# Performance work log

Hardware: AMD Instinct MI355X
Metric: run time of the kernel (lower is better)

The kernel has to match this reference:

```python
import jax, jax.numpy as jnp
import numpy as np
from jax import lax

N_G, E_G, E_LG = 100000, 400000, 1200000
N_T, E_T, E_LGT = 50000, 100000, 300000
D_F, D_MSG_G = 64, 128
VOCAB, D_EMB, D_MSG_T = 780, 128, 128
N_ITERS_G, N_ITERS_T = 4, 4
SCALE = 0.05  # keep relu/sum chains numerically tame over iterations


def setup_inputs() -> dict:
    key = jax.random.key(0)
    ks = jax.random.split(key, 32)
    f32 = jnp.float32
    w = lambda k, sh: jax.random.normal(k, sh, f32) * SCALE
    return {
        "G_f": jax.random.normal(ks[0], (N_G, D_F), f32),
        "G_ef": jax.random.normal(ks[1], (E_G, D_F), f32),
        "G_src": jax.random.randint(ks[2], (E_G,), 0, N_G, jnp.int32),
        "G_dst": jax.random.randint(ks[3], (E_G,), 0, N_G, jnp.int32),
        "G_lg_src": jax.random.randint(ks[4], (E_LG,), 0, E_G, jnp.int32),
        "G_lg_dst": jax.random.randint(ks[5], (E_LG,), 0, E_G, jnp.int32),
        "T_id": jax.random.randint(ks[6], (N_T,), 0, VOCAB, jnp.int32),
        "T_src": jax.random.randint(ks[7], (E_T,), 0, N_T, jnp.int32),
        "T_dst": jax.random.randint(ks[8], (E_T,), 0, N_T, jnp.int32),
        "T_lg_src": jax.random.randint(ks[9], (E_LGT,), 0, E_T, jnp.int32),
        "T_lg_dst": jax.random.randint(ks[10], (E_LGT,), 0, E_T, jnp.int32),
        "embeddings": jax.random.normal(ks[11], (VOCAB, D_EMB), f32),
        "W1": w(ks[12], (D_F, D_MSG_G)),
        "W2": w(ks[13], (D_F, D_MSG_G)),
        "W3": w(ks[14], (D_MSG_G, D_MSG_G)),
        "U1_G": w(ks[15], (D_F, D_MSG_G)),
        "U2_G": w(ks[16], (D_MSG_G, D_MSG_G)),
        "Wz": w(ks[17], (D_EMB, D_MSG_T)),
        "Uz": w(ks[18], (D_MSG_T, D_MSG_T)),
        "Wr": w(ks[19], (D_EMB, D_MSG_T)),
        "Ur": w(ks[20], (D_MSG_T, D_MSG_T)),
        "Wh": w(ks[21], (D_EMB, D_MSG_T)),
        "Uh": w(ks[22], (D_MSG_T, D_MSG_T)),
        "U1_T": w(ks[23], (D_EMB, D_MSG_T)),
        "U2_T": w(ks[24], (D_MSG_T, D_MSG_T)),
    }


def reference(G_f, G_ef, G_src, G_dst, G_lg_src, G_lg_dst,
              T_id, T_src, T_dst, T_lg_src, T_lg_dst,
              embeddings, W1, W2, W3, U1_G, U2_G,
              Wz, Uz, Wr, Ur, Wh, Uh, U1_T, U2_T):
    seg = jax.ops.segment_sum

    # ---- molecule graph G: loopy-BP MLP messages on the line graph ----
    f_src_G = G_f[G_src]                               # [E_G, D_F] copy_src
    base_G = f_src_G @ W1 + G_ef @ W2                  # loop-invariant part of g1_G

    def stepG(msg, _):
        sum_msg = seg(msg[G_lg_src], G_lg_dst, num_segments=E_G)
        return jax.nn.relu(base_G + sum_msg @ W3), None

    msgG0 = jnp.zeros((E_G, D_MSG_G), G_f.dtype)
    msgG, _ = lax.scan(stepG, msgG0, None, length=N_ITERS_G)

    # readout g2_G: sum edge msgs into dst nodes
    sG = seg(msgG, G_dst, num_segments=N_G)
    x_G = jax.nn.relu(G_f @ U1_G + sG @ U2_G)          # [N_G, D_MSG_G]

    # ---- junction tree T: GRU messages on the tree line graph ----
    f_T = embeddings[T_id]                             # one-hot id @ embeddings
    f_src_T = f_T[T_src]                               # [E_T, D_EMB]
    xz, xr, xh = f_src_T @ Wz, f_src_T @ Wr, f_src_T @ Wh

    def stepT(msg, _):
        s = seg(msg[T_lg_src], T_lg_dst, num_segments=E_T)
        z = jax.nn.sigmoid(xz + s @ Uz)
        r = jax.nn.sigmoid(xr + s @ Ur)
        h = jnp.tanh(xh + (r * s) @ Uh)
        return (1.0 - z) * s + z * h, None

    msgT0 = jnp.zeros((E_T, D_MSG_T), f_T.dtype)
    msgT, _ = lax.scan(stepT, msgT0, None, length=N_ITERS_T)

    sT = seg(msgT, T_dst, num_segments=N_T)
    x_T = jax.nn.relu(f_T @ U1_T + sT @ U2_T)          # [N_T, D_MSG_T]

    # concat node readouts (same width) so output is a single array
    return jnp.concatenate([x_G, x_T], axis=0)         # [N_G+N_T, 128]
```

## Files before the change

kernel.cpp:

```cpp
#include <hip/hip_runtime.h>

#define NG 100000
#define EG 400000
#define ELG 1200000
#define NT 50000
#define ET 100000
#define ELGT 300000

#define GEG ((EG + 63) / 64)
#define GET ((ET + 63) / 64)
#define GNG ((NG + 63) / 64)
#define GNT ((NT + 63) / 64)

#define SEG1 EG
#define SEG2 (EG + NG)
#define SEG3 (EG + NG + ET)
#define NSEG_ALL (EG + NG + ET + NT)
#define NE_ALL (ELG + EG + ELGT + ET)
#define NE_PAD (NE_ALL + 3 * NSEG_ALL + 64)

typedef unsigned short u16;
typedef unsigned int u32;
typedef __attribute__((ext_vector_type(8))) short bf16x8;
typedef __attribute__((ext_vector_type(4))) float f32x4;

#define TILE_B 16384

__device__ __forceinline__ float bflo(u32 p){ return __uint_as_float(p << 16); }
__device__ __forceinline__ float bfhi(u32 p){ return __uint_as_float(p & 0xffff0000u); }
__device__ __forceinline__ float bf2f(u16 h){ return __uint_as_float(((u32)h) << 16); }
__device__ __forceinline__ u16 f2bf(float f){
  u32 u = __float_as_uint(f);
  u32 r = u + 0x7fffu + ((u >> 16) & 1u);
  return (u16)(r >> 16);
}
__device__ __forceinline__ float sigm(float x){ return 1.0f / (1.0f + __expf(-x)); }
__device__ __forceinline__ float tanh_(float x){ return 2.0f / (1.0f + __expf(-2.0f * x)) - 1.0f; }
__device__ __forceinline__ float relu_(float x){ return x > 0.0f ? x : 0.0f; }
__device__ __forceinline__ void wfence(){ __builtin_amdgcn_wave_barrier(); }

__device__ __forceinline__ int swz(int r, int c){ return r * 256 + (c ^ ((r & 7) << 4)); }

__device__ __forceinline__ void zero8(float v[8]){
  #pragma unroll
  for (int j = 0; j < 8; j++) v[j] = 0.f;
}
__device__ __forceinline__ uint4 pack8(const float v[8]){
  uint4 o;
  o.x = f2bf(v[0]) | ((u32)f2bf(v[1]) << 16);
  o.y = f2bf(v[2]) | ((u32)f2bf(v[3]) << 16);
  o.z = f2bf(v[4]) | ((u32)f2bf(v[5]) << 16);
  o.w = f2bf(v[6]) | ((u32)f2bf(v[7]) << 16);
  return o;
}
__device__ __forceinline__ uint2 pack4(const f32x4& a){
  uint2 o;
  o.x = (u32)f2bf(a[0]) | ((u32)f2bf(a[1]) << 16);
  o.y = (u32)f2bf(a[2]) | ((u32)f2bf(a[3]) << 16);
  return o;
}
__device__ __forceinline__ void unp4(uint2 u, float v[4]){
  v[0] = bflo(u.x); v[1] = bfhi(u.x); v[2] = bflo(u.y); v[3] = bfhi(u.y);
}
__device__ __forceinline__ bf16x8 packfrag(const float v[8]){
  union { uint4 u; bf16x8 b; } c; c.u = pack8(v); return c.b;
}
__device__ __forceinline__ bf16x8 zfrag(){
  union { uint4 u; bf16x8 b; } c; c.u = make_uint4(0, 0, 0, 0); return c.b;
}
__device__ __forceinline__ bf16x8 as_frag(uint4 u){
  union { uint4 u; bf16x8 b; } c; c.u = u; return c.b;
}

__global__ void k_sniff(const u32* __restrict__ g, int* __restrict__ flag){
  __shared__ int sh[2];
  if (threadIdx.x < 2) sh[threadIdx.x] = 0;
  __syncthreads();
  int c0 = 0, c1 = 0;
  for (int i = 0; i < 16; i++){
    u32 w = g[threadIdx.x * 16 + i];
    u32 lo = w & 0xFFFFu;
    if (lo == 0u) c0++;
    else { u32 e = (lo >> 7) & 0xFFu; if (e >= 96u && e <= 144u) c1++; }
  }
  atomicAdd(&sh[0], c0); atomicAdd(&sh[1], c1);
  __syncthreads();
  if (threadIdx.x == 0) *flag = (sh[0] < 512 && sh[1] > 2048) ? 1 : 0;
}

__global__ void k_cvt_all(const void* p0, const void* p1, const void* p2, const void* p3,
                          const void* p4, const void* p5, const void* p6, const void* p7,
                          const void* p8, const void* p9, const void* p10, const void* p11,
                          const void* p12, float* __restrict__ wm, const int* __restrict__ flagp){
  int i = blockIdx.x * 256 + threadIdx.x;
  if (i >= 188416) return;
  const int offs[14] = {0,8192,16384,32768,40960,57344,73728,90112,106496,122880,139264,155648,172032,188416};
  const void* ps[13] = {p0,p1,p2,p3,p4,p5,p6,p7,p8,p9,p10,p11,p12};
  int w = 0;
  while (i >= offs[w + 1]) w++;
  int li = i - offs[w];
  wm[i] = (*flagp) ? bf2f(((const u16*)ps[w])[li]) : ((const float*)ps[w])[li];
}

__global__ void k_mkfrag_all(const float* __restrict__ wm, u16* __restrict__ frag){
  const int wmo[13] = {0,8192,16384,32768,40960,57344,73728,90112,106496,122880,139264,155648,172032};
  const int nks[13] = {2,2,4,2,4,4,4,4,4,4,4,4,4};
  int b = blockIdx.x;
  int wi = 0, ks = b;
  while (ks >= nks[wi]){ ks -= nks[wi]; wi++; }
  const float* W = wm + wmo[wi];
  int nt = threadIdx.x >> 6, lane = threadIdx.x & 63;
  int kr = ks * 32 + ((lane >> 4) << 3);
  int col = nt * 16 + (lane & 15);
  u16* o = frag + (size_t)b * 4096 + nt * 512 + lane * 8;
  #pragma unroll
  for (int j = 0; j < 8; j++) o[j] = f2bf(W[(size_t)(kr + j) * 128 + col]);
}

__device__ __forceinline__ const void* rowdt(const void* mat, size_t row, int W, int bf){
  return bf ? (const void*)((const u16*)mat + row * (size_t)W)
            : (const void*)((const float*)mat + row * (size_t)W);
}
__device__ __forceinline__ void load8(const void* rowbase, int c8, int bf, float v[8]){
  if (bf){
    uint4 d = ((const uint4*)rowbase)[c8];
    v[0]=bflo(d.x); v[1]=bfhi(d.x); v[2]=bflo(d.y); v[3]=bfhi(d.y);
    v[4]=bflo(d.z); v[5]=bfhi(d.z); v[6]=bflo(d.w); v[7]=bfhi(d.w);
  } else {
    const float4* p = (const float4*)rowbase + (c8 << 1);
    float4 a = p[0], b = p[1];
    v[0]=a.x; v[1]=a.y; v[2]=a.z; v[3]=a.w; v[4]=b.x; v[5]=b.y; v[6]=b.z; v[7]=b.w;
  }
}

__global__ void k_hist_all(const int* __restrict__ Glgd, const int* __restrict__ Gd,
                           const int* __restrict__ Tlgd, const int* __restrict__ Td,
                           int* __restrict__ cnt){
  int e = blockIdx.x * 256 + threadIdx.x;
  if (e >= NE_ALL) return;
  int seg;
  if (e < ELG)                       seg = Glgd[e];
  else if (e < ELG + EG)             seg = SEG1 + Gd[e - ELG];
  else if (e < ELG + EG + ELGT)      seg = SEG2 + Tlgd[e - ELG - EG];
  else                               seg = SEG3 + Td[e - ELG - EG - ELGT];
  atomicAdd(&cnt[seg], 1);
}

__global__ void k_scan1(const int* __restrict__ cnt, int n, int* __restrict__ csum){
  int base = blockIdx.x * 4096, tid = threadIdx.x;
  int s = 0;
  for (int i = 0; i < 16; i++){
    int idx = base + i * 256 + tid;
    if (idx < n) s += (cnt[idx] + 3) & ~3;
  }
  __shared__ int red[4];
  for (int off = 32; off; off >>= 1) s += __shfl_down(s, off, 64);
  if ((tid & 63) == 0) red[tid >> 6] = s;
  __syncthreads();
  if (tid == 0) csum[blockIdx.x] = red[0] + red[1] + red[2] + red[3];
}

__global__ void k_scan2(int* csum, int nch, int* rowptr, int n){
  if (threadIdx.x == 0){
    int run = 0;
    for (int c = 0; c < nch; c++){ int t = csum[c]; csum[c] = run; run += t; }
    rowptr[n] = run;
  }
}

__global__ void k_scan3(const int* __restrict__ cnt, int n, const int* __restrict__ csum,
                        int* __restrict__ rowptr){
  __shared__ int buf[4096];
  __shared__ int tsum[256];
  int base = blockIdx.x * 4096, tid = threadIdx.x;
  for (int i = 0; i < 16; i++){
    int idx = base + i * 256 + tid;
    buf[i * 256 + tid] = (idx < n) ? ((cnt[idx] + 3) & ~3) : 0;
  }
  __syncthreads();
  int run = 0;
  for (int i = 0; i < 16; i++){ int v = buf[tid * 16 + i]; buf[tid * 16 + i] = run; run += v; }
  tsum[tid] = run;
  __syncthreads();
  for (int off = 1; off < 256; off <<= 1){
    int v = (tid >= off) ? tsum[tid - off] : 0;
    __syncthreads();
    tsum[tid] += v;
    __syncthreads();
  }
  int texcl = tsum[tid] - run;
  int cbase = csum[blockIdx.x];
  for (int i = 0; i < 16; i++){
    int idx = base + tid * 16 + i;
    if (idx < n) rowptr[idx] = cbase + texcl + buf[tid * 16 + i];
  }
}

__global__ void k_fill_all(const int* __restrict__ Glgd, const int* __restrict__ Glgs,
                           const int* __restrict__ Gd,
                           const int* __restrict__ Tlgd, const int* __restrict__ Tlgs,
                           const int* __restrict__ Td,
                           const int* __restrict__ rowptr, int* __restrict__ fill,
                           int* __restrict__ col){
  int e = blockIdx.x * 256 + threadIdx.x;
  if (e >= NE_ALL) return;
  int seg, srcv;
  if (e < ELG){                      seg = Glgd[e];                           srcv = Glgs[e]; }
  else if (e < ELG + EG){            int l = e - ELG;                         seg = SEG1 + Gd[l];   srcv = l; }
  else if (e < ELG + EG + ELGT){     int l = e - ELG - EG;                    seg = SEG2 + Tlgd[l]; srcv = Tlgs[l]; }
  else {                             int l = e - ELG - EG - ELGT;             seg = SEG3 + Td[l];   srcv = l; }
  int pos = atomicAdd(&fill[seg], 1);
  col[rowptr[seg] + pos] = srcv;
}

__global__ void k_fill_pad(const int* __restrict__ cnt, const int* __restrict__ rowptr,
                           int* __restrict__ col){
  int seg = blockIdx.x * 256 + threadIdx.x;
  if (seg >= NSEG_ALL) return;
  int dummy = (seg < SEG2) ? EG : ET;
  int start = rowptr[seg] + cnt[seg];
  int end = rowptr[seg + 1];
  for (int q = start; q < end; q++) col[q] = dummy;
}

__global__ void k_zero_dummy(u16* a, u16* b, u16* c, u16* d){
  int i = threadIdx.x;
  if (i < 128){
    a[(size_t)EG * 128 + i] = 0; b[(size_t)EG * 128 + i] = 0;
    c[(size_t)ET * 128 + i] = 0; d[(size_t)ET * 128 + i] = 0;
  }
}


__device__ __forceinline__ void acc8_add(float (&a)[8], uint4 d){
  a[0] += bflo(d.x); a[1] += bfhi(d.x);
  a[2] += bflo(d.y); a[3] += bfhi(d.y);
  a[4] += bflo(d.z); a[5] += bfhi(d.z);
  a[6] += bflo(d.w); a[7] += bfhi(d.w);
}

__device__ __forceinline__ void gather_accum(const int* __restrict__ rowptr,
    const int* __restrict__ colidx, const u16* __restrict__ msg,
    int row, int M, int kg, float (&acc)[4][8])
{
  #pragma unroll
  for (int ks = 0; ks < 4; ks++) zero8(acc[ks]);
  if (row >= M) return;
  int p = rowptr[row], pe = rowptr[row + 1];
  for (; p < pe; p += 4){
    int i0 = colidx[p], i1 = colidx[p + 1], i2 = colidx[p + 2], i3 = colidx[p + 3];
    const uint4* b0 = (const uint4*)(msg + (size_t)i0 * 128);
    const uint4* b1 = (const uint4*)(msg + (size_t)i1 * 128);
    const uint4* b2 = (const uint4*)(msg + (size_t)i2 * 128);
    const uint4* b3 = (const uint4*)(msg + (size_t)i3 * 128);
    uint4 v0[4], v1[4], v2[4], v3[4];
    #pragma unroll
    for (int ks = 0; ks < 4; ks++){
      v0[ks] = b0[ks * 4 + kg]; v1[ks] = b1[ks * 4 + kg];
      v2[ks] = b2[ks * 4 + kg]; v3[ks] = b3[ks * 4 + kg];
    }
    #pragma unroll
    for (int ks = 0; ks < 4; ks++){
      acc8_add(acc[ks], v0[ks]); acc8_add(acc[ks], v1[ks]);
      acc8_add(acc[ks], v2[ks]); acc8_add(acc[ks], v3[ks]);
    }
  }
}

template<int KS>
__device__ __forceinline__ void mma_f(const bf16x8* a, const u16* __restrict__ frag,
                                      f32x4 (&acc)[8])
{
  int lane = threadIdx.x & 63;
  #pragma unroll
  for (int ks = 0; ks < KS; ks++){
    const u16* fb = frag + (size_t)ks * 4096 + lane * 8;
    #pragma unroll
    for (int nt = 0; nt < 8; nt++){
      bf16x8 b = *(const bf16x8*)(fb + (size_t)nt * 512);
      acc[nt] = __builtin_amdgcn_mfma_f32_16x16x32_bf16(a[ks], b, acc[nt], 0, 0, 0);
    }
  }
}

#define INIT_ACC(A) { _Pragma("unroll") for (int n_=0;n_<8;n_++){ A[n_][0]=0.f; A[n_][1]=0.f; A[n_][2]=0.f; A[n_][3]=0.f; } }

__device__ __forceinline__ void repack_store(const char* __restrict__ tile,
    u16* __restrict__ dst, int row0, int M)
{
  int rl = threadIdx.x >> 2, q = threadIdx.x & 3;
  int grow = row0 + rl;
  if (grow < M){
    #pragma unroll
    for (int v = 0; v < 4; v++){
      uint4 d = *(const uint4*)(tile + swz(rl, (v * 4 + q) * 16));
      *(uint4*)(dst + (size_t)grow * 128 + (size_t)(v * 4 + q) * 8) = d;
    }
  }
}

__device__ __forceinline__ size_t fslot(int blk, int w, int nt){
  return ((((size_t)blk * 4 + w) * 8 + nt) * 64 + (threadIdx.x & 63)) * 4;
}

__device__ __forceinline__ void load_catfrag(const void* __restrict__ Gf,
    const void* __restrict__ Gef, const int* __restrict__ Gsrc,
    int arow, int kg, int bf, bf16x8 (&fC)[4])
{
  if (arow < EG){
    int sr = Gsrc[arow];
    const void* ra = rowdt(Gf, (size_t)sr, 64, bf);
    const void* rb = rowdt(Gef, (size_t)arow, 64, bf);
    float t[8];
    load8(ra, kg, bf, t);     fC[0] = packfrag(t);
    load8(ra, 4 + kg, bf, t); fC[1] = packfrag(t);
    load8(rb, kg, bf, t);     fC[2] = packfrag(t);
    load8(rb, 4 + kg, bf, t); fC[3] = packfrag(t);
  } else {
    #pragma unroll
    for (int ks = 0; ks < 4; ks++) fC[ks] = zfrag();
  }
}


__global__ __launch_bounds__(256, 4) void k_init(
    const void* __restrict__ Gf, const void* __restrict__ Gef, const int* __restrict__ Gsrc,
    const u16* __restrict__ fWcat, const int* __restrict__ flagp, u16* __restrict__ msgG,
    const void* __restrict__ emb, const int* __restrict__ Tid, const int* __restrict__ Tsrc,
    const u16* __restrict__ fWz, const u16* __restrict__ fWr, const u16* __restrict__ fWh,
    u16* __restrict__ xzf, u16* __restrict__ xrf, u16* __restrict__ xhf, u16* __restrict__ msgT)
{
  __shared__ char t0[TILE_B];
  int bf = *flagp;
  int lane = threadIdx.x & 63, w = threadIdx.x >> 6;
  int stripe = w * 16, kg = lane >> 4, m16 = lane & 15;
  if (blockIdx.x < GET){
    int blk = blockIdx.x, row0 = blk * 64, arow = row0 + stripe + m16;
    bf16x8 fE[4];
    if (arow < ET){
      int id = Tid[Tsrc[arow]];
      const void* rb = rowdt(emb, (size_t)id, 128, bf);
      #pragma unroll
      for (int ks = 0; ks < 4; ks++){
        float t[8]; load8(rb, ks * 4 + kg, bf, t); fE[ks] = packfrag(t);
      }
    } else {
      #pragma unroll
      for (int ks = 0; ks < 4; ks++) fE[ks] = zfrag();
    }
    f32x4 acc[8];
    uint2 zpk[8];
    INIT_ACC(acc);
    mma_f<4>(fE, fWz, acc);
    #pragma unroll
    for (int nt = 0; nt < 8; nt++){
      zpk[nt] = pack4(acc[nt]);
      *(uint2*)(xzf + fslot(blk, w, nt)) = zpk[nt];
    }
    INIT_ACC(acc);
    mma_f<4>(fE, fWr, acc);
    #pragma unroll
    for (int nt = 0; nt < 8; nt++)
      *(uint2*)(xrf + fslot(blk, w, nt)) = pack4(acc[nt]);
    INIT_ACC(acc);
    mma_f<4>(fE, fWh, acc);
    #pragma unroll
    for (int nt = 0; nt < 8; nt++){
      *(uint2*)(xhf + fslot(blk, w, nt)) = pack4(acc[nt]);
      float xzv[4]; unp4(zpk[nt], xzv);
      #pragma unroll
      for (int r = 0; r < 4; r++){
        int rt = stripe + (kg << 2) + r;
        int cb = nt * 32 + m16 * 2;
        *(u16*)(t0 + swz(rt, cb)) = f2bf(sigm(xzv[r]) * tanh_(acc[nt][r]));
      }
    }
    wfence();
    repack_store(t0, msgT, row0, ET);
  } else {
    int blk = blockIdx.x - GET, row0 = blk * 64, arow = row0 + stripe + m16;
    bf16x8 fC[4];
    load_catfrag(Gf, Gef, Gsrc, arow, kg, bf, fC);
    f32x4 acc[8]; INIT_ACC(acc);
    mma_f<4>(fC, fWcat, acc);
    #pragma unroll
    for (int nt = 0; nt < 8; nt++)
      #pragma unroll
      for (int r = 0; r < 4; r++){
        int rt = stripe + (kg << 2) + r;
        int cb = nt * 32 + m16 * 2;
        *(u16*)(t0 + swz(rt, cb)) = f2bf(relu_(acc[nt][r]));
      }
    wfence();
    repack_store(t0, msgG, row0, EG);
  }
}

__global__ __launch_bounds__(256, 4) void k_iter(
    const u16* __restrict__ msgInG, u16* __restrict__ msgOutG,
    const void* __restrict__ Gf, const void* __restrict__ Gef, const int* __restrict__ Gsrc,
    const int* __restrict__ rp, const int* __restrict__ col,
    const u16* __restrict__ fWcat, const u16* __restrict__ fW3, const int* __restrict__ flagp,
    const u16* __restrict__ msgInT, u16* __restrict__ msgOutT,
    const u16* __restrict__ fUz, const u16* __restrict__ fUr, const u16* __restrict__ fUh,
    const u16* __restrict__ xzf, const u16* __restrict__ xrf, const u16* __restrict__ xhf)
{
  __shared__ char t0[TILE_B];
  __shared__ char t1[TILE_B];
  int lane = threadIdx.x & 63, w = threadIdx.x >> 6;
  int stripe = w * 16, kg = lane >> 4, m16 = lane & 15;
  if (blockIdx.x < GET){
    int blk = blockIdx.x, row0 = blk * 64, arow = row0 + stripe + m16;
    float ga[4][8];
    gather_accum(rp + SEG2, col, msgInT, arow, ET, kg, ga);
    bf16x8 fS[4];
    #pragma unroll
    for (int ks = 0; ks < 4; ks++){
      uint4 pk = pack8(ga[ks]);
      *(uint4*)(t0 + swz(stripe + m16, ks * 64 + kg * 16)) = pk;
      fS[ks] = as_frag(pk);
    }
    f32x4 acc[8];
    INIT_ACC(acc);
    mma_f<4>(fS, fUr, acc);
    wfence();
    #pragma unroll
    for (int nt = 0; nt < 8; nt++){
      uint2 r4 = *(const uint2*)(xrf + fslot(blk, w, nt));
      float xrv[4]; unp4(r4, xrv);
      #pragma unroll
      for (int r = 0; r < 4; r++){
        int rt = stripe + (kg << 2) + r;
        int cb = nt * 32 + m16 * 2;
        float s = bf2f(*(const u16*)(t0 + swz(rt, cb)));
        float rr = sigm(xrv[r] + acc[nt][r]);
        *(u16*)(t1 + swz(rt, cb)) = f2bf(rr * s);
      }
    }
    wfence();
    bf16x8 fRS[4];
    #pragma unroll
    for (int ks = 0; ks < 4; ks++)
      fRS[ks] = *(const bf16x8*)(t1 + swz(stripe + m16, ks * 64 + kg * 16));
    INIT_ACC(acc);
    mma_f<4>(fRS, fUh, acc);
    wfence();
    #pragma unroll
    for (int nt = 0; nt < 8; nt++){
      uint2 h4 = *(const uint2*)(xhf + fslot(blk, w, nt));
      float xhv[4]; unp4(h4, xhv);
      #pragma unroll
      for (int r = 0; r < 4; r++){
        int rt = stripe + (kg << 2) + r;
        int cb = nt * 32 + m16 * 2;
        *(u16*)(t1 + swz(rt, cb)) = f2bf(tanh_(xhv[r] + acc[nt][r]));
      }
    }
    wfence();
    bf16x8 fS2[4];
    #pragma unroll
    for (int ks = 0; ks < 4; ks++)
      fS2[ks] = *(const bf16x8*)(t0 + swz(stripe + m16, ks * 64 + kg * 16));
    INIT_ACC(acc);
    mma_f<4>(fS2, fUz, acc);
    wfence();
    #pragma unroll
    for (int nt = 0; nt < 8; nt++){
      uint2 z4 = *(const uint2*)(xzf + fslot(blk, w, nt));
      float xzv[4]; unp4(z4, xzv);
      #pragma unroll
      for (int r = 0; r < 4; r++){
        int rt = stripe + (kg << 2) + r;
        int cb = nt * 32 + m16 * 2;
        float z = sigm(xzv[r] + acc[nt][r]);
        float s = bf2f(*(const u16*)(t0 + swz(rt, cb)));
        float h = bf2f(*(const u16*)(t1 + swz(rt, cb)));
        *(u16*)(t0 + swz(rt, cb)) = f2bf((1.f - z) * s + z * h);
      }
    }
    wfence();
    repack_store(t0, msgOutT, row0, ET);
  } else {
    int bf = *flagp;
    int blk = blockIdx.x - GET, row0 = blk * 64, arow = row0 + stripe + m16;
    float ga[4][8];
    gather_accum(rp, col, msgInG, arow, EG, kg, ga);
    bf16x8 fS[4];
    #pragma unroll
    for (int ks = 0; ks < 4; ks++) fS[ks] = packfrag(ga[ks]);
    bf16x8 fC[4];
    load_catfrag(Gf, Gef, Gsrc, arow, kg, bf, fC);
    f32x4 acc[8]; INIT_ACC(acc);
    mma_f<4>(fS, fW3, acc);
    mma_f<4>(fC, fWcat, acc);
    #pragma unroll
    for (int nt = 0; nt < 8; nt++)
      #pragma unroll
      for (int r = 0; r < 4; r++){
        int rt = stripe + (kg << 2) + r;
        int cb = nt * 32 + m16 * 2;
        *(u16*)(t0 + swz(rt, cb)) = f2bf(relu_(acc[nt][r]));
      }
    wfence();
    repack_store(t0, msgOutG, row0, EG);
  }
}

__global__ __launch_bounds__(256, 4) void k_readout(
    const void* __restrict__ Gf, const u16* __restrict__ msgG,
    const int* __restrict__ rp, const int* __restrict__ col,
    const u16* __restrict__ fU1G, const u16* __restrict__ fU2G,
    const void* __restrict__ emb, const int* __restrict__ Tid, const u16* __restrict__ msgT,
    const u16* __restrict__ fU1T, const u16* __restrict__ fU2T,
    const int* __restrict__ flagp, float* __restrict__ out)
{
  int bf = *flagp;
  int lane = threadIdx.x & 63, w = threadIdx.x >> 6;
  int stripe = w * 16, kg = lane >> 4, m16 = lane & 15;
  if (blockIdx.x < GNT){
    int row0 = blockIdx.x * 64, arow = row0 + stripe + m16;
    float ga[4][8];
    gather_accum(rp + SEG3, col, msgT, arow, NT, kg, ga);
    bf16x8 fS[4];
    #pragma unroll
    for (int ks = 0; ks < 4; ks++) fS[ks] = packfrag(ga[ks]);
    bf16x8 fE[4];
    if (arow < NT){
      int id = Tid[arow];
      const void* rb = rowdt(emb, (size_t)id, 128, bf);
      #pragma unroll
      for (int ks = 0; ks < 4; ks++){
        float t[8]; load8(rb, ks * 4 + kg, bf, t); fE[ks] = packfrag(t);
      }
    } else {
      #pragma unroll
      for (int ks = 0; ks < 4; ks++) fE[ks] = zfrag();
    }
    f32x4 acc[8]; INIT_ACC(acc);
    mma_f<4>(fS, fU2T, acc);
    mma_f<4>(fE, fU1T, acc);
    #pragma unroll
    for (int nt = 0; nt < 8; nt++)
      #pragma unroll
      for (int r = 0; r < 4; r++){
        int R = row0 + stripe + (kg << 2) + r;
        if (R < NT) out[(size_t)(NG + R) * 128 + nt * 16 + m16] = relu_(acc[nt][r]);
      }
  } else {
    int row0 = (blockIdx.x - GNT) * 64, arow = row0 + stripe + m16;
    float ga[4][8];
    gather_accum(rp + SEG1, col, msgG, arow, NG, kg, ga);
    bf16x8 fS[4];
    #pragma unroll
    for (int ks = 0; ks < 4; ks++) fS[ks] = packfrag(ga[ks]);
    bf16x8 fG[2];
    if (arow < NG){
      const void* ra = rowdt(Gf, (size_t)arow, 64, bf);
      float t[8];
      load8(ra, kg, bf, t);     fG[0] = packfrag(t);
      load8(ra, 4 + kg, bf, t); fG[1] = packfrag(t);
    } else { fG[0] = zfrag(); fG[1] = zfrag(); }
    f32x4 acc[8]; INIT_ACC(acc);
    mma_f<4>(fS, fU2G, acc);
    mma_f<2>(fG, fU1G, acc);
    #pragma unroll
    for (int nt = 0; nt < 8; nt++)
      #pragma unroll
      for (int r = 0; r < 4; r++){
        int R = row0 + stripe + (kg << 2) + r;
        if (R < NG) out[(size_t)R * 128 + nt * 16 + m16] = relu_(acc[nt][r]);
      }
  }
}

extern "C" void kernel_launch(void* const* d_in, const int* in_sizes, int n_in,
                              void* d_out, int out_size, void* d_ws, size_t ws_size,
                              hipStream_t stream)
{
  const void* G_f      = d_in[0];
  const void* G_ef     = d_in[1];
  const int*  G_src    = (const int*)d_in[2];
  const int*  G_dst    = (const int*)d_in[3];
  const int*  G_lg_src = (const int*)d_in[4];
  const int*  G_lg_dst = (const int*)d_in[5];
  const int*  T_id     = (const int*)d_in[6];
  const int*  T_src    = (const int*)d_in[7];
  const int*  T_dst    = (const int*)d_in[8];
  const int*  T_lg_src = (const int*)d_in[9];
  const int*  T_lg_dst = (const int*)d_in[10];
  const void* emb      = d_in[11];
  float* out = (float*)d_out;
  (void)in_sizes; (void)n_in; (void)out_size; (void)ws_size;

  size_t off = 0;
  auto alloc = [&](size_t bytes) -> char* {
    char* p = (char*)d_ws + off;
    off += (bytes + 255) & ~(size_t)255;
    return p;
  };

  int*   flag = (int*)alloc(256);
  float* wm   = (float*)alloc(sizeof(float) * 188416);
  u16*   frag = (u16*)alloc(2 * 46 * 4096);
  const u16* fWcat = frag;
  const u16* fW3   = frag + (size_t)4  * 4096;
  const u16* fU1G  = frag + (size_t)8  * 4096;
  const u16* fU2G  = frag + (size_t)10 * 4096;
  const u16* fWz   = frag + (size_t)14 * 4096;
  const u16* fUz   = frag + (size_t)18 * 4096;
  const u16* fWr   = frag + (size_t)22 * 4096;
  const u16* fUr   = frag + (size_t)26 * 4096;
  const u16* fWh   = frag + (size_t)30 * 4096;
  const u16* fUh   = frag + (size_t)34 * 4096;
  const u16* fU1T  = frag + (size_t)38 * 4096;
  const u16* fU2T  = frag + (size_t)42 * 4096;

  int* rp   = (int*)alloc(sizeof(int) * (NSEG_ALL + 1));
  int* col  = (int*)alloc(sizeof(int) * NE_PAD);
  int* cnt  = (int*)alloc(sizeof(int) * 2 * NSEG_ALL);
  int* csum = (int*)alloc(sizeof(int) * 256);
  u16* msgGA = (u16*)alloc((size_t)(EG + 1) * 128 * 2);
  u16* msgGB = (u16*)alloc((size_t)(EG + 1) * 128 * 2);
  u16* xzf   = (u16*)alloc((size_t)GET * 8192 * 2);
  u16* xrf   = (u16*)alloc((size_t)GET * 8192 * 2);
  u16* xhf   = (u16*)alloc((size_t)GET * 8192 * 2);
  u16* msgTA = (u16*)alloc((size_t)(ET + 1) * 128 * 2);
  u16* msgTB = (u16*)alloc((size_t)(ET + 1) * 128 * 2);

  k_sniff<<<1, 256, 0, stream>>>((const u32*)G_ef, flag);
  k_cvt_all<<<(188416 + 255) / 256, 256, 0, stream>>>(
      d_in[12], d_in[13], d_in[14], d_in[15], d_in[16], d_in[17], d_in[18],
      d_in[19], d_in[20], d_in[21], d_in[22], d_in[23], d_in[24], wm, flag);
  k_mkfrag_all<<<46, 512, 0, stream>>>(wm, frag);
  k_zero_dummy<<<1, 128, 0, stream>>>(msgGA, msgGB, msgTA, msgTB);

  hipMemsetAsync(cnt, 0, sizeof(int) * 2 * NSEG_ALL, stream);
  k_hist_all<<<(NE_ALL + 255) / 256, 256, 0, stream>>>(G_lg_dst, G_dst, T_lg_dst, T_dst, cnt);
  int nch = (NSEG_ALL + 4095) / 4096;
  k_scan1<<<nch, 256, 0, stream>>>(cnt, NSEG_ALL, csum);
  k_scan2<<<1, 64, 0, stream>>>(csum, nch, rp, NSEG_ALL);
  k_scan3<<<nch, 256, 0, stream>>>(cnt, NSEG_ALL, csum, rp);
  k_fill_all<<<(NE_ALL + 255) / 256, 256, 0, stream>>>(
      G_lg_dst, G_lg_src, G_dst, T_lg_dst, T_lg_src, T_dst, rp, cnt + NSEG_ALL, col);
  k_fill_pad<<<(NSEG_ALL + 255) / 256, 256, 0, stream>>>(cnt, rp, col);

  k_init<<<GET + GEG, 256, 0, stream>>>(G_f, G_ef, G_src, fWcat, flag, msgGA,
                                        emb, T_id, T_src, fWz, fWr, fWh, xzf, xrf, xhf, msgTA);
  k_iter<<<GET + GEG, 256, 0, stream>>>(msgGA, msgGB, G_f, G_ef, G_src, rp, col, fWcat, fW3, flag,
                                        msgTA, msgTB, fUz, fUr, fUh, xzf, xrf, xhf);
  k_iter<<<GET + GEG, 256, 0, stream>>>(msgGB, msgGA, G_f, G_ef, G_src, rp, col, fWcat, fW3, flag,
                                        msgTB, msgTA, fUz, fUr, fUh, xzf, xrf, xhf);
  k_iter<<<GET + GEG, 256, 0, stream>>>(msgGA, msgGB, G_f, G_ef, G_src, rp, col, fWcat, fW3, flag,
                                        msgTA, msgTB, fUz, fUr, fUh, xzf, xrf, xhf);
  k_readout<<<GNT + GNG, 256, 0, stream>>>(G_f, msgGB, rp, col, fU1G, fU2G,
                                           emb, T_id, msgTB, fU1T, fU2T, flag, out);
}
```

Before: 1.098 ms.

## Fold neighbor-sum gather into MFMA via distributivity; cut shared tile and use nontemporal stores

```diff
diff --git a/kernel.cpp b/kernel.cpp
--- a/kernel.cpp
+++ b/kernel.cpp
@@ -23,6 +23,7 @@
 typedef unsigned int u32;
 typedef __attribute__((ext_vector_type(8))) short bf16x8;
 typedef __attribute__((ext_vector_type(4))) float f32x4;
+typedef __attribute__((ext_vector_type(4))) u32 u32x4;
 
 #define TILE_B 16384
 
@@ -39,20 +40,13 @@
 __device__ __forceinline__ float relu_(float x){ return x > 0.0f ? x : 0.0f; }
 __device__ __forceinline__ void wfence(){ __builtin_amdgcn_wave_barrier(); }
 
+__device__ __forceinline__ void stnt4(void* p, uint4 d){
+  u32x4 v = {d.x, d.y, d.z, d.w};
+  __builtin_nontemporal_store(v, (u32x4*)p);
+}
+
 __device__ __forceinline__ int swz(int r, int c){ return r * 256 + (c ^ ((r & 7) << 4)); }
 
-__device__ __forceinline__ void zero8(float v[8]){
-  #pragma unroll
-  for (int j = 0; j < 8; j++) v[j] = 0.f;
-}
-__device__ __forceinline__ uint4 pack8(const float v[8]){
-  uint4 o;
-  o.x = f2bf(v[0]) | ((u32)f2bf(v[1]) << 16);
-  o.y = f2bf(v[2]) | ((u32)f2bf(v[3]) << 16);
-  o.z = f2bf(v[4]) | ((u32)f2bf(v[5]) << 16);
-  o.w = f2bf(v[6]) | ((u32)f2bf(v[7]) << 16);
-  return o;
-}
 __device__ __forceinline__ uint2 pack4(const f32x4& a){
   uint2 o;
   o.x = (u32)f2bf(a[0]) | ((u32)f2bf(a[1]) << 16);
@@ -62,14 +56,25 @@
 __device__ __forceinline__ void unp4(uint2 u, float v[4]){
   v[0] = bflo(u.x); v[1] = bfhi(u.x); v[2] = bflo(u.y); v[3] = bfhi(u.y);
 }
-__device__ __forceinline__ bf16x8 packfrag(const float v[8]){
-  union { uint4 u; bf16x8 b; } c; c.u = pack8(v); return c.b;
+__device__ __forceinline__ uint2 pack4a(const float v[4]){
+  uint2 o;
+  o.x = (u32)f2bf(v[0]) | ((u32)f2bf(v[1]) << 16);
+  o.y = (u32)f2bf(v[2]) | ((u32)f2bf(v[3]) << 16);
+  return o;
 }
 __device__ __forceinline__ bf16x8 zfrag(){
   union { uint4 u; bf16x8 b; } c; c.u = make_uint4(0, 0, 0, 0); return c.b;
 }
 __device__ __forceinline__ bf16x8 as_frag(uint4 u){
   union { uint4 u; bf16x8 b; } c; c.u = u; return c.b;
+}
+__device__ __forceinline__ bf16x8 packfrag(const float v[8]){
+  union { uint4 u; bf16x8 b; } c;
+  c.u.x = f2bf(v[0]) | ((u32)f2bf(v[1]) << 16);
+  c.u.y = f2bf(v[2]) | ((u32)f2bf(v[3]) << 16);
+  c.u.z = f2bf(v[4]) | ((u32)f2bf(v[5]) << 16);
+  c.u.w = f2bf(v[6]) | ((u32)f2bf(v[7]) << 16);
+  return c.b;
 }
 
 __global__ void k_sniff(const u32* __restrict__ g, int* __restrict__ flag){
@@ -115,6 +120,16 @@
   u16* o = frag + (size_t)b * 4096 + nt * 512 + lane * 8;
   #pragma unroll
   for (int j = 0; j < 8; j++) o[j] = f2bf(W[(size_t)(kr + j) * 128 + col]);
+}
+
+__global__ void k_mkident(u16* __restrict__ fI){
+  int ks = blockIdx.x;
+  int nt = threadIdx.x >> 6, lane = threadIdx.x & 63;
+  int kr = ks * 32 + ((lane >> 4) << 3);
+  int col = nt * 16 + (lane & 15);
+  u16* o = fI + (size_t)ks * 4096 + nt * 512 + lane * 8;
+  #pragma unroll
+  for (int j = 0; j < 8; j++) o[j] = (kr + j == col) ? (u16)0x3F80 : (u16)0;
 }
 
 __device__ __forceinline__ const void* rowdt(const void* mat, size_t row, int W, int bf){
@@ -231,38 +246,36 @@
   }
 }
 
-
-__device__ __forceinline__ void acc8_add(float (&a)[8], uint4 d){
-  a[0] += bflo(d.x); a[1] += bfhi(d.x);
-  a[2] += bflo(d.y); a[3] += bfhi(d.y);
-  a[4] += bflo(d.z); a[5] += bfhi(d.z);
-  a[6] += bflo(d.w); a[7] += bfhi(d.w);
-}
-
-__device__ __forceinline__ void gather_accum(const int* __restrict__ rowptr,
+__device__ __forceinline__ void gather_mma(const int* __restrict__ rowptr,
     const int* __restrict__ colidx, const u16* __restrict__ msg,
-    int row, int M, int kg, float (&acc)[4][8])
-{
-  #pragma unroll
-  for (int ks = 0; ks < 4; ks++) zero8(acc[ks]);
-  if (row >= M) return;
-  int p = rowptr[row], pe = rowptr[row + 1];
-  for (; p < pe; p += 4){
-    int i0 = colidx[p], i1 = colidx[p + 1], i2 = colidx[p + 2], i3 = colidx[p + 3];
+    int row, int M, int kg, int dummy, const u16* __restrict__ frag,
+    f32x4 (&acc)[8])
+{
+  int lane = threadIdx.x & 63;
+  const u16* fbase = frag + lane * 8;
+  int p0 = 0, pe = 0;
+  if (row < M){ p0 = rowptr[row]; pe = rowptr[row + 1]; }
+  for (int sl = 0; __any(p0 + sl < pe); sl += 2){
+    uint2 ci = *(const uint2*)(colidx + p0 + sl);
+    int i0 = (p0 + sl     < pe) ? (int)ci.x : dummy;
+    int i1 = (p0 + sl + 1 < pe) ? (int)ci.y : dummy;
     const uint4* b0 = (const uint4*)(msg + (size_t)i0 * 128);
     const uint4* b1 = (const uint4*)(msg + (size_t)i1 * 128);
-    const uint4* b2 = (const uint4*)(msg + (size_t)i2 * 128);
-    const uint4* b3 = (const uint4*)(msg + (size_t)i3 * 128);
-    uint4 v0[4], v1[4], v2[4], v3[4];
+    bf16x8 a0[4], a1[4];
     #pragma unroll
     for (int ks = 0; ks < 4; ks++){
-      v0[ks] = b0[ks * 4 + kg]; v1[ks] = b1[ks * 4 + kg];
-      v2[ks] = b2[ks * 4 + kg]; v3[ks] = b3[ks * 4 + kg];
+      a0[ks] = as_frag(b0[ks * 4 + kg]);
+      a1[ks] = as_frag(b1[ks * 4 + kg]);
     }
     #pragma unroll
     for (int ks = 0; ks < 4; ks++){
-      acc8_add(acc[ks], v0[ks]); acc8_add(acc[ks], v1[ks]);
-      acc8_add(acc[ks], v2[ks]); acc8_add(acc[ks], v3[ks]);
+      const u16* fb = fbase + (size_t)ks * 4096;
+      #pragma unroll
+      for (int nt = 0; nt < 8; nt++){
+        bf16x8 b = *(const bf16x8*)(fb + (size_t)nt * 512);
+        acc[nt] = __builtin_amdgcn_mfma_f32_16x16x32_bf16(a0[ks], b, acc[nt], 0, 0, 0);
+        acc[nt] = __builtin_amdgcn_mfma_f32_16x16x32_bf16(a1[ks], b, acc[nt], 0, 0, 0);
+      }
     }
   }
 }
@@ -294,7 +307,7 @@
     #pragma unroll
     for (int v = 0; v < 4; v++){
       uint4 d = *(const uint4*)(tile + swz(rl, (v * 4 + q) * 16));
-      *(uint4*)(dst + (size_t)grow * 128 + (size_t)(v * 4 + q) * 8) = d;
+      stnt4(dst + (size_t)grow * 128 + (size_t)(v * 4 + q) * 8, d);
     }
   }
 }
@@ -403,79 +416,80 @@
     const u16* __restrict__ fWcat, const u16* __restrict__ fW3, const int* __restrict__ flagp,
     const u16* __restrict__ msgInT, u16* __restrict__ msgOutT,
     const u16* __restrict__ fUz, const u16* __restrict__ fUr, const u16* __restrict__ fUh,
+    const u16* __restrict__ fI,
     const u16* __restrict__ xzf, const u16* __restrict__ xrf, const u16* __restrict__ xhf)
 {
   __shared__ char t0[TILE_B];
-  __shared__ char t1[TILE_B];
   int lane = threadIdx.x & 63, w = threadIdx.x >> 6;
   int stripe = w * 16, kg = lane >> 4, m16 = lane & 15;
   if (blockIdx.x < GET){
     int blk = blockIdx.x, row0 = blk * 64, arow = row0 + stripe + m16;
-    float ga[4][8];
-    gather_accum(rp + SEG2, col, msgInT, arow, ET, kg, ga);
-    bf16x8 fS[4];
-    #pragma unroll
-    for (int ks = 0; ks < 4; ks++){
-      uint4 pk = pack8(ga[ks]);
-      *(uint4*)(t0 + swz(stripe + m16, ks * 64 + kg * 16)) = pk;
-      fS[ks] = as_frag(pk);
-    }
     f32x4 acc[8];
     INIT_ACC(acc);
-    mma_f<4>(fS, fUr, acc);
-    wfence();
+    gather_mma(rp + SEG2, col, msgInT, arow, ET, kg, ET, fI, acc);
+    uint2 spk[8];
     #pragma unroll
     for (int nt = 0; nt < 8; nt++){
-      uint2 r4 = *(const uint2*)(xrf + fslot(blk, w, nt));
-      float xrv[4]; unp4(r4, xrv);
+      spk[nt] = pack4(acc[nt]);
       #pragma unroll
       for (int r = 0; r < 4; r++){
         int rt = stripe + (kg << 2) + r;
         int cb = nt * 32 + m16 * 2;
-        float s = bf2f(*(const u16*)(t0 + swz(rt, cb)));
+        *(u16*)(t0 + swz(rt, cb)) = f2bf(acc[nt][r]);
+      }
+    }
+    wfence();
+    bf16x8 fS[4];
+    #pragma unroll
+    for (int ks = 0; ks < 4; ks++)
+      fS[ks] = *(const bf16x8*)(t0 + swz(stripe + m16, ks * 64 + kg * 16));
+    INIT_ACC(acc);
+    mma_f<4>(fS, fUr, acc);
+    wfence();
+    #pragma unroll
+    for (int nt = 0; nt < 8; nt++){
+      uint2 xr4 = *(const uint2*)(xrf + fslot(blk, w, nt));
+      float xrv[4], sv[4];
+      unp4(xr4, xrv); unp4(spk[nt], sv);
+      #pragma unroll
+      for (int r = 0; r < 4; r++){
+        int rt = stripe + (kg << 2) + r;
+        int cb = nt * 32 + m16 * 2;
         float rr = sigm(xrv[r] + acc[nt][r]);
-        *(u16*)(t1 + swz(rt, cb)) = f2bf(rr * s);
-      }
-    }
-    wfence();
+        *(u16*)(t0 + swz(rt, cb)) = f2bf(rr * sv[r]);
+      }
+    }
+    wfence();
+    INIT_ACC(acc);
+    mma_f<4>(fS, fUz, acc);
+    uint2 zpk[8];
+    #pragma unroll
+    for (int nt = 0; nt < 8; nt++){
+      uint2 xz4 = *(const uint2*)(xzf + fslot(blk, w, nt));
+      float xzv[4], zv[4];
+      unp4(xz4, xzv);
+      #pragma unroll
+      for (int r = 0; r < 4; r++) zv[r] = sigm(xzv[r] + acc[nt][r]);
+      zpk[nt] = pack4a(zv);
+    }
     bf16x8 fRS[4];
     #pragma unroll
     for (int ks = 0; ks < 4; ks++)
-      fRS[ks] = *(const bf16x8*)(t1 + swz(stripe + m16, ks * 64 + kg * 16));
+      fRS[ks] = *(const bf16x8*)(t0 + swz(stripe + m16, ks * 64 + kg * 16));
     INIT_ACC(acc);
     mma_f<4>(fRS, fUh, acc);
     wfence();
     #pragma unroll
     for (int nt = 0; nt < 8; nt++){
-      uint2 h4 = *(const uint2*)(xhf + fslot(blk, w, nt));
-      float xhv[4]; unp4(h4, xhv);
+      uint2 xh4 = *(const uint2*)(xhf + fslot(blk, w, nt));
+      float xhv[4], sv[4], zv[4];
+      unp4(xh4, xhv); unp4(spk[nt], sv); unp4(zpk[nt], zv);
       #pragma unroll
       for (int r = 0; r < 4; r++){
         int rt = stripe + (kg << 2) + r;
         int cb = nt * 32 + m16 * 2;
-        *(u16*)(t1 + swz(rt, cb)) = f2bf(tanh_(xhv[r] + acc[nt][r]));
-      }
-    }
-    wfence();
-    bf16x8 fS2[4];
-    #pragma unroll
-    for (int ks = 0; ks < 4; ks++)
-      fS2[ks] = *(const bf16x8*)(t0 + swz(stripe + m16, ks * 64 + kg * 16));
-    INIT_ACC(acc);
-    mma_f<4>(fS2, fUz, acc);
-    wfence();
-    #pragma unroll
-    for (int nt = 0; nt < 8; nt++){
-      uint2 z4 = *(const uint2*)(xzf + fslot(blk, w, nt));
-      float xzv[4]; unp4(z4, xzv);
-      #pragma unroll
-      for (int r = 0; r < 4; r++){
-        int rt = stripe + (kg << 2) + r;
-        int cb = nt * 32 + m16 * 2;
-        float z = sigm(xzv[r] + acc[nt][r]);
-        float s = bf2f(*(const u16*)(t0 + swz(rt, cb)));
-        float h = bf2f(*(const u16*)(t1 + swz(rt, cb)));
-        *(u16*)(t0 + swz(rt, cb)) = f2bf((1.f - z) * s + z * h);
+        float h = tanh_(xhv[r] + acc[nt][r]);
+        *(u16*)(t0 + swz(rt, cb)) = f2bf((1.f - zv[r]) * sv[r] + zv[r] * h);
       }
     }
     wfence();
@@ -483,15 +497,10 @@
   } else {
     int bf = *flagp;
     int blk = blockIdx.x - GET, row0 = blk * 64, arow = row0 + stripe + m16;
-    float ga[4][8];
-    gather_accum(rp, col, msgInG, arow, EG, kg, ga);
-    bf16x8 fS[4];
-    #pragma unroll
-    for (int ks = 0; ks < 4; ks++) fS[ks] = packfrag(ga[ks]);
+    f32x4 acc[8]; INIT_ACC(acc);
+    gather_mma(rp, col, msgInG, arow, EG, kg, EG, fW3, acc);
     bf16x8 fC[4];
     load_catfrag(Gf, Gef, Gsrc, arow, kg, bf, fC);
-    f32x4 acc[8]; INIT_ACC(acc);
-    mma_f<4>(fS, fW3, acc);
     mma_f<4>(fC, fWcat, acc);
     #pragma unroll
     for (int nt = 0; nt < 8; nt++)
@@ -519,11 +528,8 @@
   int stripe = w * 16, kg = lane >> 4, m16 = lane & 15;
   if (blockIdx.x < GNT){
     int row0 = blockIdx.x * 64, arow = row0 + stripe + m16;
-    float ga[4][8];
-    gather_accum(rp + SEG3, col, msgT, arow, NT, kg, ga);
-    bf16x8 fS[4];
-    #pragma unroll
-    for (int ks = 0; ks < 4; ks++) fS[ks] = packfrag(ga[ks]);
+    f32x4 acc[8]; INIT_ACC(acc);
+    gather_mma(rp + SEG3, col, msgT, arow, NT, kg, ET, fU2T, acc);
     bf16x8 fE[4];
     if (arow < NT){
       int id = Tid[arow];
@@ -536,23 +542,19 @@
       #pragma unroll
       for (int ks = 0; ks < 4; ks++) fE[ks] = zfrag();
     }
-    f32x4 acc[8]; INIT_ACC(acc);
-    mma_f<4>(fS, fU2T, acc);
     mma_f<4>(fE, fU1T, acc);
     #pragma unroll
     for (int nt = 0; nt < 8; nt++)
       #pragma unroll
       for (int r = 0; r < 4; r++){
         int R = row0 + stripe + (kg << 2) + r;
-        if (R < NT) out[(size_t)(NG + R) * 128 + nt * 16 + m16] = relu_(acc[nt][r]);
+        if (R < NT) __builtin_nontemporal_store(relu_(acc[nt][r]),
+                        &out[(size_t)(NG + R) * 128 + nt * 16 + m16]);
       }
   } else {
     int row0 = (blockIdx.x - GNT) * 64, arow = row0 + stripe + m16;
-    float ga[4][8];
-    gather_accum(rp + SEG1, col, msgG, arow, NG, kg, ga);
-    bf16x8 fS[4];
-    #pragma unroll
-    for (int ks = 0; ks < 4; ks++) fS[ks] = packfrag(ga[ks]);
+    f32x4 acc[8]; INIT_ACC(acc);
+    gather_mma(rp + SEG1, col, msgG, arow, NG, kg, EG, fU2G, acc);
     bf16x8 fG[2];
     if (arow < NG){
       const void* ra = rowdt(Gf, (size_t)arow, 64, bf);
@@ -560,15 +562,14 @@
       load8(ra, kg, bf, t);     fG[0] = packfrag(t);
       load8(ra, 4 + kg, bf, t); fG[1] = packfrag(t);
     } else { fG[0] = zfrag(); fG[1] = zfrag(); }
-    f32x4 acc[8]; INIT_ACC(acc);
-    mma_f<4>(fS, fU2G, acc);
     mma_f<2>(fG, fU1G, acc);
     #pragma unroll
     for (int nt = 0; nt < 8; nt++)
       #pragma unroll
       for (int r = 0; r < 4; r++){
         int R = row0 + stripe + (kg << 2) + r;
-        if (R < NG) out[(size_t)R * 128 + nt * 16 + m16] = relu_(acc[nt][r]);
+        if (R < NG) __builtin_nontemporal_store(relu_(acc[nt][r]),
+                        &out[(size_t)R * 128 + nt * 16 + m16]);
       }
   }
 }
@@ -602,6 +603,7 @@
   int*   flag = (int*)alloc(256);
   float* wm   = (float*)alloc(sizeof(float) * 188416);
   u16*   frag = (u16*)alloc(2 * 46 * 4096);
+  u16*   fI   = (u16*)alloc(2 * 4 * 4096);
   const u16* fWcat = frag;
   const u16* fW3   = frag + (size_t)4  * 4096;
   const u16* fU1G  = frag + (size_t)8  * 4096;
@@ -632,6 +634,7 @@
       d_in[12], d_in[13], d_in[14], d_in[15], d_in[16], d_in[17], d_in[18],
       d_in[19], d_in[20], d_in[21], d_in[22], d_in[23], d_in[24], wm, flag);
   k_mkfrag_all<<<46, 512, 0, stream>>>(wm, frag);
+  k_mkident<<<4, 512, 0, stream>>>(fI);
   k_zero_dummy<<<1, 128, 0, stream>>>(msgGA, msgGB, msgTA, msgTB);
 
   hipMemsetAsync(cnt, 0, sizeof(int) * 2 * NSEG_ALL, stream);
@@ -647,11 +650,11 @@
   k_init<<<GET + GEG, 256, 0, stream>>>(G_f, G_ef, G_src, fWcat, flag, msgGA,
                                         emb, T_id, T_src, fWz, fWr, fWh, xzf, xrf, xhf, msgTA);
   k_iter<<<GET + GEG, 256, 0, stream>>>(msgGA, msgGB, G_f, G_ef, G_src, rp, col, fWcat, fW3, flag,
-                                        msgTA, msgTB, fUz, fUr, fUh, xzf, xrf, xhf);
+                                        msgTA, msgTB, fUz, fUr, fUh, fI, xzf, xrf, xhf);
   k_iter<<<GET + GEG, 256, 0, stream>>>(msgGB, msgGA, G_f, G_ef, G_src, rp, col, fWcat, fW3, flag,
-                                        msgTB, msgTA, fUz, fUr, fUh, xzf, xrf, xhf);
+                                        msgTB, msgTA, fUz, fUr, fUh, fI, xzf, xrf, xhf);
   k_iter<<<GET + GEG, 256, 0, stream>>>(msgGA, msgGB, G_f, G_ef, G_src, rp, col, fWcat, fW3, flag,
-                                        msgTA, msgTB, fUz, fUr, fUh, xzf, xrf, xhf);
+                                        msgTA, msgTB, fUz, fUr, fUh, fI, xzf, xrf, xhf);
   k_readout<<<GNT + GNG, 256, 0, stream>>>(G_f, msgGB, rp, col, fU1G, fU2G,
                                            emb, T_id, msgTB, fU1T, fU2T, flag, out);
 }
```

New measurement: 3.044 ms. 2.77x slower.
